# Kernel optimization log

Hardware: AMD Instinct MI355X
Metric: run time of the kernel (lower is better)

Reference implementation:

```python
import jax, jax.numpy as jnp
import numpy as np

K, N = 8192, 8192
GROUP_SIZE = 128
N_GROUPS = N // GROUP_SIZE  # 64
NBITS = 4
B, T = 8, 32


def setup_inputs() -> dict:
    key = jax.random.key(0)
    k_x, k_q, k_s, k_z, k_m1, k_m2, k_b = jax.random.split(key, 7)
    x = jax.random.normal(k_x, (B, T, N), dtype=jnp.float32)
    # int8 quantized weight codes in [0, 2**nbits - 1]
    W_q = jax.random.randint(k_q, (K, N), 0, 2 ** NBITS, dtype=jnp.int32)
    # group-wise scales/zeros, shaped for broadcast against [K, n_groups, group_size]
    scales = jax.random.uniform(k_s, (K, N_GROUPS, 1), dtype=jnp.float32, minval=0.01, maxval=0.1)
    zeros = jax.random.uniform(k_z, (K, N_GROUPS, 1), dtype=jnp.float32, minval=0.0, maxval=2.0 ** NBITS - 1.0)
    # Sinkhorn row/col scaling factors (positive, near 1)
    mu1 = jnp.exp(0.1 * jax.random.normal(k_m1, (N,), dtype=jnp.float32))
    mu2 = jnp.exp(0.1 * jax.random.normal(k_m2, (K,), dtype=jnp.float32))
    bias = jax.random.normal(k_b, (K,), dtype=jnp.float32)
    return {"x": x, "W_q": W_q, "scales": scales, "zeros": zeros,
            "mu1": mu1, "mu2": mu2, "bias": bias}


def reference(x, W_q, scales, zeros, mu1, mu2, bias):
    k, n = W_q.shape
    n_groups = scales.shape[1]
    group_size = n // n_groups
    # group-wise dequant: (Q - zero) * scale, then Sinkhorn row/col rescale
    Q_g = W_q.astype(jnp.float32).reshape(k, n_groups, group_size)
    W_deq = ((Q_g - zeros) * scales).reshape(k, n)
    W_deq = W_deq * mu2[:, None] * mu1[None, :]
    W_deq = W_deq.astype(x.dtype)
    # nn.functional.linear: x @ W^T + b ; x: [B, T, N] -> [B, T, K]
    out = jnp.einsum('btn,kn->btk', x, W_deq) + bias
    return out
```

## Files before the change

### kernel.cpp

```cpp
#include <hip/hip_runtime.h>
#include <hip/hip_bf16.h>

#define M_DIM 256
#define K_DIM 8192
#define N_DIM 8192
#define NGRP  64

#define BN 128
#define BK 32
#define THREADS 512
#define SPLITN 8
#define CHUNK  (N_DIM / SPLITN)
#define NSTEPS (CHUNK / BK)
#define NG     (CHUNK >> 7)

#define ASIZE 16384
#define BSIZE 8192
#define B_OFF  (3 * ASIZE)
#define SL_OFF (3 * ASIZE + BSIZE)
#define LDS_TOTAL (SL_OFF + NG * 128 * 8)

typedef __bf16 bf16x8 __attribute__((ext_vector_type(8)));
typedef __bf16 bf16x4 __attribute__((ext_vector_type(4)));
typedef float  f32x4  __attribute__((ext_vector_type(4)));

#define SW(a) ((a) ^ ((((a) >> 7) & 7) << 4))

#define GLOAD_LDS16(g, l) __builtin_amdgcn_global_load_lds( \
    (const __attribute__((address_space(1))) void*)(g),     \
    (__attribute__((address_space(3))) void*)(l), 16, 0, 0)

__global__ __launch_bounds__(256) void prep_xs(const float* __restrict__ x,
                                               const float* __restrict__ mu1,
                                               __bf16* __restrict__ xs) {
    int t  = blockIdx.x * 256 + threadIdx.x;
    int n4 = t & 2047;
    int m  = t >> 11;
    int n  = n4 << 2;
    float4 xv = *(const float4*)(x + (size_t)m * N_DIM + n);
    float4 mv = *(const float4*)(mu1 + n);
    bf16x4 o;
    o[0] = (__bf16)(xv.x * mv.x);
    o[1] = (__bf16)(xv.y * mv.y);
    o[2] = (__bf16)(xv.z * mv.z);
    o[3] = (__bf16)(xv.w * mv.w);
    *(bf16x4*)(xs + (size_t)m * N_DIM + n) = o;
}

__global__ __launch_bounds__(THREADS, 4)
void gemm_q(const __bf16* __restrict__ xs, const int* __restrict__ Wq,
            const float* __restrict__ scales, const float* __restrict__ zeros,
            __bf16* __restrict__ partial) {
    extern __shared__ __align__(1024) char lds[];

    const int b     = blockIdx.x;
    const int split = b & 7;
    const int kidx  = b >> 3;
    const int k0    = kidx * BN;
    const int nbase = split * CHUNK;
    const int gbase = split * NG;

    const int tid  = threadIdx.x;
    const int lane = tid & 63;
    const int w    = tid >> 6;
    const int wm   = w >> 2;
    const int wn   = w & 3;
    const int start = kidx & (NSTEPS - 1);

    float* SL = (float*)(lds + SL_OFF);

    {
        int r = tid >> 2, gq = tid & 3;
#pragma unroll
        for (int gg = 0; gg < (NG >> 2); ++gg) {
            int g = (gg << 2) | gq;
            size_t si = (size_t)(k0 + r) * NGRP + gbase + g;
            float s = scales[si];
            float z = zeros[si];
            float2 v; v.x = s; v.y = -z * s;
            *(float2*)&SL[(size_t)((g << 7) + r) * 2] = v;
        }
    }

    const char* asrc[2];
    int aoff[2];
#pragma unroll
    for (int cc = 0; cc < 2; ++cc) {
        int c   = w * 2 + cc;
        int off = c * 1024 + lane * 16;
        int L   = SW(off);
        aoff[cc] = off;
        asrc[cc] = (const char*)xs + ((size_t)(L >> 6) * N_DIM) * 2 + (L & 63);
    }

    const int brow = w * 16 + (lane >> 2);
    const int bq   = lane & 3;
    const int* bptr0 = Wq + (size_t)(k0 + brow) * N_DIM + bq * 8;
    char* bdst = lds + B_OFF + brow * 64 + bq * 16;

#define ISSUE_A(t)                                                        \
    {                                                                     \
        int s_ = ((t) + start) & (NSTEPS - 1);                            \
        char* bs_ = lds + ((t) % 3) * ASIZE;                              \
        size_t so_ = (size_t)(nbase + s_ * BK) * 2;                       \
        GLOAD_LDS16(asrc[0] + so_, bs_ + aoff[0]);                        \
        GLOAD_LDS16(asrc[1] + so_, bs_ + aoff[1]);                        \
    }
#define LOAD_B(t, q0, q1)                                                 \
    {                                                                     \
        int s_ = ((t) + start) & (NSTEPS - 1);                            \
        const int* p_ = bptr0 + (nbase + s_ * BK);                        \
        q0 = *(const int4*)p_;                                            \
        q1 = *(const int4*)(p_ + 4);                                      \
    }

    f32x4 acc[8][2];
#pragma unroll
    for (int i = 0; i < 8; ++i) {
        acc[i][0] = (f32x4){0.f, 0.f, 0.f, 0.f};
        acc[i][1] = (f32x4){0.f, 0.f, 0.f, 0.f};
    }

    int4 qa0, qa1, qb0, qb1;

    LOAD_B(0, qa0, qa1);
    ISSUE_A(0);
    asm volatile("" ::: "memory");
    LOAD_B(1, qb0, qb1);
    ISSUE_A(1);

#define STEP(it, q0c, q1c)                                                \
    {                                                                     \
        if ((it) < NSTEPS - 1) asm volatile("s_waitcnt vmcnt(4)" ::: "memory"); \
        else                   asm volatile("s_waitcnt vmcnt(0)" ::: "memory"); \
        __builtin_amdgcn_s_barrier();   \
        int scur_ = ((it) + start) & (NSTEPS - 1);                        \
        float2 sz_ = *(float2*)&SL[(size_t)(((scur_ >> 2) << 7) + brow) * 2]; \
        bf16x8 wv_;                                                       \
        wv_[0] = (__bf16)((float)q0c.x * sz_.x + sz_.y);                  \
        wv_[1] = (__bf16)((float)q0c.y * sz_.x + sz_.y);                  \
        wv_[2] = (__bf16)((float)q0c.z * sz_.x + sz_.y);                  \
        wv_[3] = (__bf16)((float)q0c.w * sz_.x + sz_.y);                  \
        wv_[4] = (__bf16)((float)q1c.x * sz_.x + sz_.y);                  \
        wv_[5] = (__bf16)((float)q1c.y * sz_.x + sz_.y);                  \
        wv_[6] = (__bf16)((float)q1c.z * sz_.x + sz_.y);                  \
        wv_[7] = (__bf16)((float)q1c.w * sz_.x + sz_.y);                  \
        *(bf16x8*)bdst = wv_;                                             \
        asm volatile("s_waitcnt lgkmcnt(0)" ::: "memory");                \
        __builtin_amdgcn_s_barrier();          \
        if ((it) + 2 < NSTEPS) {                                          \
            LOAD_B((it) + 2, q0c, q1c);                                   \
            ISSUE_A((it) + 2);                                            \
        }                                                                 \
        const char* bufA_ = lds + ((it) % 3) * ASIZE;                     \
        const char* bufB_ = lds + B_OFF;                                  \
        bf16x8 bv_[2];                                                    \
        _Pragma("unroll")                                                 \
        for (int ci = 0; ci < 2; ++ci) {                                  \
            int r_ = wn * 32 + ci * 16 + (lane & 15);                     \
            bv_[ci] = *(const bf16x8*)(bufB_ + r_ * 64 + (lane >> 4) * 16); \
        }                                                                 \
        _Pragma("unroll")                                                 \
        for (int mi = 0; mi < 8; ++mi) {                                  \
            int la_ = (wm * 128 + mi * 16 + (lane & 15)) * 64 + (lane >> 4) * 16; \
            bf16x8 av_ = *(const bf16x8*)(bufA_ + SW(la_));               \
            acc[mi][0] = __builtin_amdgcn_mfma_f32_16x16x32_bf16(av_, bv_[0], acc[mi][0], 0, 0, 0); \
            acc[mi][1] = __builtin_amdgcn_mfma_f32_16x16x32_bf16(av_, bv_[1], acc[mi][1], 0, 0, 0); \
        }                                                                 \
    }

    for (int it = 0; it < NSTEPS; it += 2) {
        STEP(it,     qa0, qa1);
        STEP(it + 1, qb0, qb1);
    }
#undef STEP
#undef ISSUE_A
#undef LOAD_B

    __bf16* outp = partial + (size_t)split * ((size_t)M_DIM * K_DIM);
#pragma unroll
    for (int mi = 0; mi < 8; ++mi) {
#pragma unroll
        for (int ci = 0; ci < 2; ++ci) {
            int gk = k0 + wn * 32 + ci * 16 + (lane & 15);
            int gm = wm * 128 + mi * 16 + (lane >> 4) * 4;
#pragma unroll
            for (int rix = 0; rix < 4; ++rix)
                outp[(size_t)(gm + rix) * K_DIM + gk] = (__bf16)acc[mi][ci][rix];
        }
    }
}

__global__ __launch_bounds__(256) void reduce_out(const __bf16* __restrict__ partial,
                                                  const float* __restrict__ mu2,
                                                  const float* __restrict__ bias,
                                                  float* __restrict__ out) {
    int t  = blockIdx.x * 256 + threadIdx.x;
    int k4 = t & 2047;
    int m  = t >> 11;
    size_t base = (size_t)m * K_DIM + (size_t)k4 * 4;
    float4 s; s.x = 0.f; s.y = 0.f; s.z = 0.f; s.w = 0.f;
#pragma unroll
    for (int sp = 0; sp < SPLITN; ++sp) {
        bf16x4 p = *(const bf16x4*)(partial + (size_t)sp * ((size_t)M_DIM * K_DIM) + base);
        s.x += (float)p[0]; s.y += (float)p[1]; s.z += (float)p[2]; s.w += (float)p[3];
    }
    float4 m2 = *(const float4*)(mu2 + (size_t)k4 * 4);
    float4 bi = *(const float4*)(bias + (size_t)k4 * 4);
    float4 o;
    o.x = s.x * m2.x + bi.x;
    o.y = s.y * m2.y + bi.y;
    o.z = s.z * m2.z + bi.z;
    o.w = s.w * m2.w + bi.w;
    *(float4*)(out + base) = o;
}

extern "C" void kernel_launch(void* const* d_in, const int* in_sizes, int n_in,
                              void* d_out, int out_size, void* d_ws, size_t ws_size,
                              hipStream_t stream) {
    const float* x      = (const float*)d_in[0];
    const int*   Wq     = (const int*)d_in[1];
    const float* scales = (const float*)d_in[2];
    const float* zeros  = (const float*)d_in[3];
    const float* mu1    = (const float*)d_in[4];
    const float* mu2    = (const float*)d_in[5];
    const float* bias   = (const float*)d_in[6];
    float* out = (float*)d_out;

    __bf16* xs = (__bf16*)d_ws;
    const size_t xs_bytes = (size_t)M_DIM * N_DIM * sizeof(__bf16);
    __bf16* partial = (__bf16*)((char*)d_ws + xs_bytes);

    (void)hipFuncSetAttribute((const void*)gemm_q,
                              hipFuncAttributeMaxDynamicSharedMemorySize,
                              LDS_TOTAL);

    prep_xs<<<2048, 256, 0, stream>>>(x, mu1, xs);
    gemm_q<<<64 * SPLITN, THREADS, LDS_TOTAL, stream>>>(xs, Wq, scales, zeros, partial);
    reduce_out<<<2048, 256, 0, stream>>>(partial, mu2, bias, out);
}
```

Baseline: 89.77 us.

## Dequantize weights directly into MFMA B-operand registers, dropping LDS staging

Each wave now owns 16 output columns across all 256 rows. It loads the int weights in the MFMA B-operand lane layout, dequantizes them in registers and feeds them straight to the MFMA. This removes the B tile LDS write, the lgkmcnt wait, the second barrier per step, and the B LDS reads. The scale/zero pair is reloaded only when the group changes. In exchange, each wave now reads all 16 A fragments from LDS per step instead of 8, which doubles A LDS traffic per wave.

```diff
diff --git a/kernel.cpp b/kernel.cpp
--- a/kernel.cpp
+++ b/kernel.cpp
@@ -15,9 +15,7 @@
 #define NG     (CHUNK >> 7)
 
 #define ASIZE 16384
-#define BSIZE 8192
-#define B_OFF  (3 * ASIZE)
-#define SL_OFF (3 * ASIZE + BSIZE)
+#define SL_OFF (3 * ASIZE)
 #define LDS_TOTAL (SL_OFF + NG * 128 * 8)
 
 typedef __bf16 bf16x8 __attribute__((ext_vector_type(8)));
@@ -63,8 +61,6 @@
     const int tid  = threadIdx.x;
     const int lane = tid & 63;
     const int w    = tid >> 6;
-    const int wm   = w >> 2;
-    const int wn   = w & 3;
     const int start = kidx & (NSTEPS - 1);
 
     float* SL = (float*)(lds + SL_OFF);
@@ -93,10 +89,8 @@
         asrc[cc] = (const char*)xs + ((size_t)(L >> 6) * N_DIM) * 2 + (L & 63);
     }
 
-    const int brow = w * 16 + (lane >> 2);
-    const int bq   = lane & 3;
-    const int* bptr0 = Wq + (size_t)(k0 + brow) * N_DIM + bq * 8;
-    char* bdst = lds + B_OFF + brow * 64 + bq * 16;
+    const int browL = w * 16 + (lane & 15);
+    const int* bptr0 = Wq + (size_t)(k0 + browL) * N_DIM + (lane >> 4) * 8;
 
 #define ISSUE_A(t)                                                        \
     {                                                                     \
@@ -114,12 +108,10 @@
         q1 = *(const int4*)(p_ + 4);                                      \
     }
 
-    f32x4 acc[8][2];
-#pragma unroll
-    for (int i = 0; i < 8; ++i) {
-        acc[i][0] = (f32x4){0.f, 0.f, 0.f, 0.f};
-        acc[i][1] = (f32x4){0.f, 0.f, 0.f, 0.f};
-    }
+    f32x4 acc[16];
+#pragma unroll
+    for (int i = 0; i < 16; ++i)
+        acc[i] = (f32x4){0.f, 0.f, 0.f, 0.f};
 
     int4 qa0, qa1, qb0, qb1;
 
@@ -128,44 +120,39 @@
     asm volatile("" ::: "memory");
     LOAD_B(1, qb0, qb1);
     ISSUE_A(1);
+    asm volatile("s_waitcnt lgkmcnt(0)" ::: "memory");
+
+    float sc = 0.f, zs = 0.f;
 
 #define STEP(it, q0c, q1c)                                                \
     {                                                                     \
         if ((it) < NSTEPS - 1) asm volatile("s_waitcnt vmcnt(4)" ::: "memory"); \
         else                   asm volatile("s_waitcnt vmcnt(0)" ::: "memory"); \
-        __builtin_amdgcn_s_barrier();   \
+        __builtin_amdgcn_s_barrier();      \
         int scur_ = ((it) + start) & (NSTEPS - 1);                        \
-        float2 sz_ = *(float2*)&SL[(size_t)(((scur_ >> 2) << 7) + brow) * 2]; \
-        bf16x8 wv_;                                                       \
-        wv_[0] = (__bf16)((float)q0c.x * sz_.x + sz_.y);                  \
-        wv_[1] = (__bf16)((float)q0c.y * sz_.x + sz_.y);                  \
-        wv_[2] = (__bf16)((float)q0c.z * sz_.x + sz_.y);                  \
-        wv_[3] = (__bf16)((float)q0c.w * sz_.x + sz_.y);                  \
-        wv_[4] = (__bf16)((float)q1c.x * sz_.x + sz_.y);                  \
-        wv_[5] = (__bf16)((float)q1c.y * sz_.x + sz_.y);                  \
-        wv_[6] = (__bf16)((float)q1c.z * sz_.x + sz_.y);                  \
-        wv_[7] = (__bf16)((float)q1c.w * sz_.x + sz_.y);                  \
-        *(bf16x8*)bdst = wv_;                                             \
-        asm volatile("s_waitcnt lgkmcnt(0)" ::: "memory");                \
-        __builtin_amdgcn_s_barrier();          \
+        if ((scur_ & 3) == 0 || (it) == 0) {                              \
+            float2 v_ = *(float2*)&SL[(size_t)(((scur_ >> 2) << 7) + browL) * 2]; \
+            sc = v_.x; zs = v_.y;                                         \
+        }                                                                 \
+        bf16x8 bv_;                                                       \
+        bv_[0] = (__bf16)((float)q0c.x * sc + zs);                        \
+        bv_[1] = (__bf16)((float)q0c.y * sc + zs);                        \
+        bv_[2] = (__bf16)((float)q0c.z * sc + zs);                        \
+        bv_[3] = (__bf16)((float)q0c.w * sc + zs);                        \
+        bv_[4] = (__bf16)((float)q1c.x * sc + zs);                        \
+        bv_[5] = (__bf16)((float)q1c.y * sc + zs);                        \
+        bv_[6] = (__bf16)((float)q1c.z * sc + zs);                        \
+        bv_[7] = (__bf16)((float)q1c.w * sc + zs);                        \
         if ((it) + 2 < NSTEPS) {                                          \
             LOAD_B((it) + 2, q0c, q1c);                                   \
             ISSUE_A((it) + 2);                                            \
         }                                                                 \
         const char* bufA_ = lds + ((it) % 3) * ASIZE;                     \
-        const char* bufB_ = lds + B_OFF;                                  \
-        bf16x8 bv_[2];                                                    \
         _Pragma("unroll")                                                 \
-        for (int ci = 0; ci < 2; ++ci) {                                  \
-            int r_ = wn * 32 + ci * 16 + (lane & 15);                     \
-            bv_[ci] = *(const bf16x8*)(bufB_ + r_ * 64 + (lane >> 4) * 16); \
-        }                                                                 \
-        _Pragma("unroll")                                                 \
-        for (int mi = 0; mi < 8; ++mi) {                                  \
-            int la_ = (wm * 128 + mi * 16 + (lane & 15)) * 64 + (lane >> 4) * 16; \
+        for (int mi = 0; mi < 16; ++mi) {                                 \
+            int la_ = (mi * 16 + (lane & 15)) * 64 + (lane >> 4) * 16;    \
             bf16x8 av_ = *(const bf16x8*)(bufA_ + SW(la_));               \
-            acc[mi][0] = __builtin_amdgcn_mfma_f32_16x16x32_bf16(av_, bv_[0], acc[mi][0], 0, 0, 0); \
-            acc[mi][1] = __builtin_amdgcn_mfma_f32_16x16x32_bf16(av_, bv_[1], acc[mi][1], 0, 0, 0); \
+            acc[mi] = __builtin_amdgcn_mfma_f32_16x16x32_bf16(av_, bv_, acc[mi], 0, 0, 0); \
         }                                                                 \
     }
 
@@ -178,16 +165,13 @@
 #undef LOAD_B
 
     __bf16* outp = partial + (size_t)split * ((size_t)M_DIM * K_DIM);
-#pragma unroll
-    for (int mi = 0; mi < 8; ++mi) {
-#pragma unroll
-        for (int ci = 0; ci < 2; ++ci) {
-            int gk = k0 + wn * 32 + ci * 16 + (lane & 15);
-            int gm = wm * 128 + mi * 16 + (lane >> 4) * 4;
-#pragma unroll
-            for (int rix = 0; rix < 4; ++rix)
-                outp[(size_t)(gm + rix) * K_DIM + gk] = (__bf16)acc[mi][ci][rix];
-        }
+    const int gk = k0 + w * 16 + (lane & 15);
+#pragma unroll
+    for (int mi = 0; mi < 16; ++mi) {
+        int gm = mi * 16 + (lane >> 4) * 4;
+#pragma unroll
+        for (int rix = 0; rix < 4; ++rix)
+            outp[(size_t)(gm + rix) * K_DIM + gk] = (__bf16)acc[mi][rix];
     }
 }
 
```

After: 103.0 us. 1.15x slower.

## Double-buffer dequantized B tile and cut to one barrier per k-step

Applied to the files above, without the earlier changes.

Double-buffers the dequantized weight tile in LDS so each k-step needs one barrier instead of two, and reorders A prefetch to one step ahead with rotating buffer pointers. It also applies XOR swizzling to the B tile to reduce LDS bank conflicts, raises wave priority around the MFMA block, and peels the last two iterations with tuned vmcnt waits. The goal is less barrier stall and more overlap of global loads with MFMA work. In exchange it uses more LDS, and the hand-counted waitcnt values make the pipeline easy to break.

```diff
diff --git a/kernel.cpp b/kernel.cpp
--- a/kernel.cpp
+++ b/kernel.cpp
@@ -17,7 +17,7 @@
 #define ASIZE 16384
 #define BSIZE 8192
 #define B_OFF  (3 * ASIZE)
-#define SL_OFF (3 * ASIZE + BSIZE)
+#define SL_OFF (B_OFF + 2 * BSIZE)
 #define LDS_TOTAL (SL_OFF + NG * 128 * 8)
 
 typedef __bf16 bf16x8 __attribute__((ext_vector_type(8)));
@@ -81,6 +81,8 @@
             *(float2*)&SL[(size_t)((g << 7) + r) * 2] = v;
         }
     }
+    asm volatile("s_waitcnt vmcnt(0) lgkmcnt(0)" ::: "memory");
+    __builtin_amdgcn_s_barrier();
 
     const char* asrc[2];
     int aoff[2];
@@ -96,15 +98,21 @@
     const int brow = w * 16 + (lane >> 2);
     const int bq   = lane & 3;
     const int* bptr0 = Wq + (size_t)(k0 + brow) * N_DIM + bq * 8;
-    char* bdst = lds + B_OFF + brow * 64 + bq * 16;
-
-#define ISSUE_A(t)                                                        \
+    char* bdst0 = lds + B_OFF + SW(brow * 64 + bq * 16);
+
+    const int rboff0 = SW((wn * 32 + 0  + (lane & 15)) * 64 + (lane >> 4) * 16);
+    const int rboff1 = SW((wn * 32 + 16 + (lane & 15)) * 64 + (lane >> 4) * 16);
+
+    char* pA0 = lds;
+    char* pA1 = lds + ASIZE;
+    char* pA2 = lds + 2 * ASIZE;
+
+#define ISSUE_A(t, pbuf)                                                  \
     {                                                                     \
         int s_ = ((t) + start) & (NSTEPS - 1);                            \
-        char* bs_ = lds + ((t) % 3) * ASIZE;                              \
         size_t so_ = (size_t)(nbase + s_ * BK) * 2;                       \
-        GLOAD_LDS16(asrc[0] + so_, bs_ + aoff[0]);                        \
-        GLOAD_LDS16(asrc[1] + so_, bs_ + aoff[1]);                        \
+        GLOAD_LDS16(asrc[0] + so_, (pbuf) + aoff[0]);                     \
+        GLOAD_LDS16(asrc[1] + so_, (pbuf) + aoff[1]);                     \
     }
 #define LOAD_B(t, q0, q1)                                                 \
     {                                                                     \
@@ -124,16 +132,14 @@
     int4 qa0, qa1, qb0, qb1;
 
     LOAD_B(0, qa0, qa1);
-    ISSUE_A(0);
+    asm volatile("" ::: "memory");
+    ISSUE_A(0, pA0);
     asm volatile("" ::: "memory");
     LOAD_B(1, qb0, qb1);
-    ISSUE_A(1);
-
-#define STEP(it, q0c, q1c)                                                \
+
+#define STEP(it, q0c, q1c, W1, W4, DO_A, DO_B)                            \
     {                                                                     \
-        if ((it) < NSTEPS - 1) asm volatile("s_waitcnt vmcnt(4)" ::: "memory"); \
-        else                   asm volatile("s_waitcnt vmcnt(0)" ::: "memory"); \
-        __builtin_amdgcn_s_barrier();   \
+        asm volatile("s_waitcnt vmcnt(" #W1 ")" ::: "memory");            \
         int scur_ = ((it) + start) & (NSTEPS - 1);                        \
         float2 sz_ = *(float2*)&SL[(size_t)(((scur_ >> 2) << 7) + brow) * 2]; \
         bf16x8 wv_;                                                       \
@@ -145,34 +151,34 @@
         wv_[5] = (__bf16)((float)q1c.y * sz_.x + sz_.y);                  \
         wv_[6] = (__bf16)((float)q1c.z * sz_.x + sz_.y);                  \
         wv_[7] = (__bf16)((float)q1c.w * sz_.x + sz_.y);                  \
-        *(bf16x8*)bdst = wv_;                                             \
-        asm volatile("s_waitcnt lgkmcnt(0)" ::: "memory");                \
-        __builtin_amdgcn_s_barrier();          \
-        if ((it) + 2 < NSTEPS) {                                          \
-            LOAD_B((it) + 2, q0c, q1c);                                   \
-            ISSUE_A((it) + 2);                                            \
-        }                                                                 \
-        const char* bufA_ = lds + ((it) % 3) * ASIZE;                     \
-        const char* bufB_ = lds + B_OFF;                                  \
-        bf16x8 bv_[2];                                                    \
-        _Pragma("unroll")                                                 \
-        for (int ci = 0; ci < 2; ++ci) {                                  \
-            int r_ = wn * 32 + ci * 16 + (lane & 15);                     \
-            bv_[ci] = *(const bf16x8*)(bufB_ + r_ * 64 + (lane >> 4) * 16); \
-        }                                                                 \
+        *(bf16x8*)(bdst0 + ((it) & 1) * BSIZE) = wv_;                     \
+        if (DO_A) { ISSUE_A((it) + 1, pA1); }                             \
+        asm volatile("" ::: "memory");                                    \
+        if (DO_B) { LOAD_B((it) + 2, q0c, q1c); }                         \
+        asm volatile("s_waitcnt vmcnt(" #W4 ") lgkmcnt(0)" ::: "memory"); \
+        __builtin_amdgcn_s_barrier();                                     \
+        const char* bufA_ = pA0;                                          \
+        const char* bufB_ = lds + B_OFF + ((it) & 1) * BSIZE;             \
+        bf16x8 bv0_ = *(const bf16x8*)(bufB_ + rboff0);                   \
+        bf16x8 bv1_ = *(const bf16x8*)(bufB_ + rboff1);                   \
+        __builtin_amdgcn_s_setprio(1);                                    \
         _Pragma("unroll")                                                 \
         for (int mi = 0; mi < 8; ++mi) {                                  \
             int la_ = (wm * 128 + mi * 16 + (lane & 15)) * 64 + (lane >> 4) * 16; \
             bf16x8 av_ = *(const bf16x8*)(bufA_ + SW(la_));               \
-            acc[mi][0] = __builtin_amdgcn_mfma_f32_16x16x32_bf16(av_, bv_[0], acc[mi][0], 0, 0, 0); \
-            acc[mi][1] = __builtin_amdgcn_mfma_f32_16x16x32_bf16(av_, bv_[1], acc[mi][1], 0, 0, 0); \
+            acc[mi][0] = __builtin_amdgcn_mfma_f32_16x16x32_bf16(av_, bv0_, acc[mi][0], 0, 0, 0); \
+            acc[mi][1] = __builtin_amdgcn_mfma_f32_16x16x32_bf16(av_, bv1_, acc[mi][1], 0, 0, 0); \
         }                                                                 \
-    }
-
-    for (int it = 0; it < NSTEPS; it += 2) {
-        STEP(it,     qa0, qa1);
-        STEP(it + 1, qb0, qb1);
-    }
+        __builtin_amdgcn_s_setprio(0);                                    \
+        { char* t_ = pA0; pA0 = pA1; pA1 = pA2; pA2 = t_; }               \
+    }
+
+    for (int it = 0; it < NSTEPS - 2; it += 2) {
+        STEP(it,     qa0, qa1, 4, 6, true, true);
+        STEP(it + 1, qb0, qb1, 4, 6, true, true);
+    }
+    STEP(NSTEPS - 2, qa0, qa1, 4, 4, true,  false);
+    STEP(NSTEPS - 1, qb0, qb1, 2, 0, false, false);
 #undef STEP
 #undef ISSUE_A
 #undef LOAD_B
```

After: 89.50 us. About the same (-0.3%).
